# Performance work log

Hardware: AMD Instinct MI355X
Metric: run time of the kernel (lower is better)

## Reference

```python
import jax, jax.numpy as jnp
import numpy as np
import math
from jax import lax

# cfg['MODEL'] constants
MU = 0.1          # FISTA step size
LMBD = 0.1        # LAMBDA[0], sparsity weight
N_DICT = 1        # EXPANSION_FACTOR
N_STEPS = 6       # NUM_LAYERS (FISTA iterations)
K = 3             # kernel_size
PAD = 1           # padding
STRIDE = 1        # stride (POOLING=False, stride passed to conv)
DN = ('NCHW', 'OIHW', 'NCHW')


def _conv(x, w):
    # F.conv2d(x, w, stride=1, padding=PAD)
    return lax.conv_general_dilated(x, w, (STRIDE, STRIDE), [(PAD, PAD), (PAD, PAD)], dimension_numbers=DN)


def _conv_t(y, w):
    # F.conv_transpose2d(y, w, stride=1, padding=PAD) == conv2d with flipped, in/out-swapped kernel, pad K-1-PAD
    wt = jnp.transpose(jnp.flip(w, (-1, -2)), (1, 0, 2, 3))  # [Cin, Cout, K, K]
    p = K - 1 - PAD
    return lax.conv_general_dilated(y, wt, (1, 1), [(p, p), (p, p)], dimension_numbers=DN)


def _shrink(z, thr):
    # non_negative=True soft-threshold: relu(z - thr)
    return jax.nn.relu(z - thr)


def setup_inputs() -> dict:
    key = jax.random.key(0)
    k1, k2 = jax.random.split(key)
    x = jax.random.normal(k1, (16, 64, 56, 56), dtype=jnp.float32)
    # dictionary weight [out_channels, in_channels*n_dict, K, K], kaiming-ish scale
    W = jax.random.normal(k2, (128, 64 * N_DICT, K, K), dtype=jnp.float32) * 0.05
    return {"x": x, "W": W}


def reference(x, W):
    # w_norm: each output filter normalized to unit Frobenius norm
    Wn = W / jnp.sqrt(jnp.sum(W * W, axis=(1, 2, 3), keepdims=True) + 1e-12)
    thr = MU * LMBD
    xr = jnp.tile(x, (1, N_DICT, 1, 1)) if N_DICT > 1 else x

    # FISTA iteration 0: c = shrink(mu * D^T x)
    c = _shrink(MU * _conv(xr, Wn), thr)
    y = c
    c_prev = c
    t = 1.0
    for _ in range(N_STEPS - 1):
        r = xr - _conv_t(y, Wn)                       # residual x - D c
        c_new = _shrink(y + MU * _conv(r, Wn), thr)   # gradient step + shrink
        t_next = (1.0 + math.sqrt(1.0 + 4.0 * t * t)) / 2.0
        y = c_new + ((t - 1.0) / t_next) * (c_new - c_prev)  # momentum
        c_prev = c_new
        t = t_next
    # POOLING=False -> DictConv2d returns the sparse code directly
    return c_prev
```

## Files before the change

kernel.cpp:

```cpp
#include <hip/hip_runtime.h>
#include <hip/hip_bf16.h>
#include <math.h>

typedef __attribute__((ext_vector_type(8))) short short8;
typedef __attribute__((ext_vector_type(16))) float f32x16;

#define MU_  0.1f
#define THR_ 0.01f

static __device__ inline short f2bf(float f) {
    __hip_bfloat16 h = __float2bfloat16(f);
    return *reinterpret_cast<short*>(&h);
}
static __device__ inline float bf2f(unsigned short u) {
    unsigned int x = ((unsigned int)u) << 16;
    return __builtin_bit_cast(float, x);
}

__global__ __launch_bounds__(256) void zero_kernel(float4* p, int n4) {
    int i = blockIdx.x * 256 + threadIdx.x;
    if (i < n4) p[i] = make_float4(0.f, 0.f, 0.f, 0.f);
}

__global__ __launch_bounds__(64) void wnorm_pack(
    const float* __restrict__ W, short* __restrict__ Wf, short* __restrict__ Wt) {
    int co = blockIdx.x, ci = threadIdx.x;
    const float* wp = W + (co * 64 + ci) * 9;
    float v[9]; float s = 0.f;
#pragma unroll
    for (int t = 0; t < 9; ++t) { v[t] = wp[t]; s += v[t] * v[t]; }
#pragma unroll
    for (int off = 32; off; off >>= 1) s += __shfl_xor(s, off, 64);
    float inv = 1.0f / sqrtf(s + 1e-12f);
#pragma unroll
    for (int t = 0; t < 9; ++t) {
        Wf[(t * 128 + co) * 64 + (ci ^ ((co & 7) << 3))] = f2bf(v[t] * inv);
        Wt[(t * 64 + ci) * 128 + (co ^ ((ci & 7) << 3))] = f2bf(v[8 - t] * inv);
    }
}

__global__ __launch_bounds__(256) void pack_x(
    const float* __restrict__ x, short* __restrict__ Xp) {
    __shared__ float lx[64 * 57];
    int row = blockIdx.x, n = blockIdx.y, tid = threadIdx.x;
    short* dst = Xp + ((size_t)(n * 58 + row) * 68) * 64;
    if (row >= 1 && row <= 56) {
        int h = row - 1;
        for (int j = tid; j < 64 * 56; j += 256) {
            int ci = j / 56, w = j - ci * 56;
            lx[ci * 57 + w] = x[((size_t)(n * 64 + ci)) * 3136 + h * 56 + w];
        }
        __syncthreads();
        for (int j = tid; j < 68 * 64; j += 256) {
            int s = j >> 6, ci = j & 63;
            float val = (s >= 2 && s < 58) ? lx[ci * 57 + (s - 2)] : 0.f;
            dst[(s << 6) + (ci ^ ((s & 7) << 3))] = f2bf(val);
        }
    } else {
        for (int j = tid; j < 68 * 64; j += 256) dst[j] = 0;
    }
}

__global__ __launch_bounds__(256) void conv_fwd(
    const short* __restrict__ inp,
    const short* __restrict__ Wf,
    short* __restrict__ Yp,
    short* __restrict__ Cp,
    float* __restrict__ outp, int mode, float beta) {
    __shared__ short xs[3 * 68 * 64];
    const int r = blockIdx.x + 1, cb = blockIdx.y, n = blockIdx.z, tid = threadIdx.x;
    {
        const short8* src = (const short8*)(inp + ((size_t)(n * 58 + (r - 1)) * 68) * 64);
        short8* d = (short8*)xs;
        for (int j = tid; j < 1632; j += 256) d[j] = src[j];
    }

    const size_t prow = ((size_t)(n * 58 + r) * 68) * 128;
    short8 yold8[2], cold8[2];
    int pvv[2], pg[2]; bool pok[2];
#pragma unroll
    for (int k = 0; k < 2; ++k) {
        int item = tid + k * 256;
        pok[k] = item < 448;
        pvv[k] = item >> 3; pg[k] = item & 7;
        if (mode != 0 && pok[k]) {
            int s = pvv[k] + 2;
            size_t off = prow + (size_t)s * 128 + 8 * ((pg[k] + 8 * cb) ^ (s & 7));
            yold8[k] = *(const short8*)(Yp + off);
            if (mode == 1) cold8[k] = *(const short8*)(Cp + off);
        }
    }
    __syncthreads();

    const int lane = tid & 63, wid = tid >> 6, qh = lane >> 5, v0 = lane & 31;
    const int ms = wid & 1, ph = wid >> 1;
    const int co = cb * 64 + ms * 32 + v0;
    const int v  = ph * 32 + v0;
    const int h  = r - 1;

    int goffA[4], bg[3][4];
#pragma unroll
    for (int s = 0; s < 4; ++s) goffA[s] = 8 * ((2 * s + qh) ^ (v0 & 7));
#pragma unroll
    for (int dw = 0; dw < 3; ++dw) {
        int key = (v0 + dw + 1) & 7;
#pragma unroll
        for (int s = 0; s < 4; ++s) bg[dw][s] = 8 * ((2 * s + qh) ^ key);
    }
    const short* wbase = Wf + co * 64;

    f32x16 acc;
#pragma unroll
    for (int i = 0; i < 16; ++i) acc[i] = 0.f;

    short8 Af[2][4];
#pragma unroll
    for (int s = 0; s < 4; ++s) Af[0][s] = *(const short8*)(wbase + goffA[s]);

#pragma unroll
    for (int t = 0; t < 9; ++t) {
        if (t + 1 < 9) {
#pragma unroll
            for (int s = 0; s < 4; ++s)
                Af[(t + 1) & 1][s] = *(const short8*)(wbase + (t + 1) * 8192 + goffA[s]);
        }
        const int dh = t / 3, dw = t % 3;
        const int b_base = (dh * 68 + (v + dw + 1)) * 64;
#pragma unroll
        for (int s = 0; s < 4; ++s) {
            short8 bv = *(const short8*)(xs + b_base + bg[dw][s]);
            acc = __builtin_amdgcn_mfma_f32_32x32x16_bf16(Af[t & 1][s], bv, acc, 0, 0, 0);
        }
    }

    __syncthreads();
    short* tb_y = xs;
    short* tb_c = xs + 4608;
    if (mode != 0) {
#pragma unroll
        for (int k = 0; k < 2; ++k) if (pok[k]) {
            int o = pvv[k] * 72 + 8 * (pg[k] ^ (pvv[k] & 3));
            *(short8*)(tb_y + o) = yold8[k];
            if (mode == 1) *(short8*)(tb_c + o) = cold8[k];
        }
    }
    __syncthreads();
#pragma unroll
    for (int reg = 0; reg < 16; ++reg) {
        const int crl = (reg & 3) + 8 * (reg >> 2) + 4 * qh;
        const int lch = ms * 32 + crl;
        const int slot = v * 72 + (lch ^ ((v & 3) << 3));
        const float a = acc[reg];
        if (mode == 0) {
            float c = fmaxf(MU_ * a - THR_, 0.f);
            short cb16 = f2bf(c);
            tb_y[slot] = cb16;
            tb_c[slot] = cb16;
        } else if (mode == 1) {
            float yold = bf2f((unsigned short)tb_y[slot]);
            float cold = bf2f((unsigned short)tb_c[slot]);
            float c = fmaxf(yold + MU_ * a - THR_, 0.f);
            float ynew = c + beta * (c - cold);
            tb_y[slot] = f2bf(ynew);
            tb_c[slot] = f2bf(c);
        } else {
            if (v < 56) {
                float yold = bf2f((unsigned short)tb_y[slot]);
                float c = fmaxf(yold + MU_ * a - THR_, 0.f);
                outp[((size_t)(n * 128 + cb * 64 + lch)) * 3136 + h * 56 + v] = c;
            }
        }
    }
    if (mode != 2) {
        __syncthreads();
        short* ydst = Yp + prow;
        short* cdst = Cp + prow;
        for (int item = tid; item < 448; item += 256) {
            int vv = item >> 3, g = item & 7;
            int so = vv * 72 + 8 * (g ^ (vv & 3));
            short8 yv = *(const short8*)(tb_y + so);
            short8 cv = *(const short8*)(tb_c + so);
            int s = vv + 2;
            size_t off = (size_t)s * 128 + 8 * ((g + 8 * cb) ^ (s & 7));
            *(short8*)(ydst + off) = yv;
            *(short8*)(cdst + off) = cv;
        }
    }
}

__global__ __launch_bounds__(256) void conv_t(
    const short* __restrict__ Ypb,
    const short* __restrict__ Wt,
    const short* __restrict__ Xp,
    short* __restrict__ Rp) {
    __shared__ short ys[3 * 68 * 128];
    const int r = blockIdx.x + 1, n = blockIdx.y, tid = threadIdx.x;
    {
        const short8* src = (const short8*)(Ypb + ((size_t)(n * 58 + (r - 1)) * 68) * 128);
        short8* d = (short8*)ys;
        for (int j = tid; j < 3264; j += 256) d[j] = src[j];
    }

    const size_t prow = ((size_t)(n * 58 + r) * 68) * 64;
    short8 xold8[2];
    int pvv[2], pg[2]; bool pok[2];
#pragma unroll
    for (int k = 0; k < 2; ++k) {
        int item = tid + k * 256;
        pok[k] = item < 448;
        pvv[k] = item >> 3; pg[k] = item & 7;
        if (pok[k]) {
            int s = pvv[k] + 2;
            xold8[k] = *(const short8*)(Xp + prow + (size_t)s * 64 + 8 * (pg[k] ^ (s & 7)));
        }
    }
    __syncthreads();

    const int lane = tid & 63, wid = tid >> 6, qh = lane >> 5, l31 = lane & 31;
    const int cib = (wid & 1) * 32, vb = (wid >> 1) * 32;
    const int ci = cib + l31;
    const int v = vb + l31;

    int goffA[8], bg[3][8];
#pragma unroll
    for (int s = 0; s < 8; ++s) goffA[s] = 8 * ((2 * s + qh) ^ (ci & 7));
#pragma unroll
    for (int dw = 0; dw < 3; ++dw) {
        int key = (l31 + dw + 1) & 7;
#pragma unroll
        for (int s = 0; s < 8; ++s) bg[dw][s] = 8 * ((2 * s + qh) ^ key);
    }
    const short* wbase = Wt + ci * 128;

    f32x16 acc;
#pragma unroll
    for (int i = 0; i < 16; ++i) acc[i] = 0.f;

    short8 Af[2][8];
#pragma unroll
    for (int s = 0; s < 8; ++s) Af[0][s] = *(const short8*)(wbase + goffA[s]);

#pragma unroll
    for (int t = 0; t < 9; ++t) {
        if (t + 1 < 9) {
#pragma unroll
            for (int s = 0; s < 8; ++s)
                Af[(t + 1) & 1][s] = *(const short8*)(wbase + (t + 1) * 8192 + goffA[s]);
        }
        const int dh = t / 3, dw = t % 3;
        const int b_base = (dh * 68 + (v + dw + 1)) * 128;
#pragma unroll
        for (int s = 0; s < 8; ++s) {
            short8 bv = *(const short8*)(ys + b_base + bg[dw][s]);
            acc = __builtin_amdgcn_mfma_f32_32x32x16_bf16(Af[t & 1][s], bv, acc, 0, 0, 0);
        }
    }

    __syncthreads();
    short* tb = ys;
#pragma unroll
    for (int k = 0; k < 2; ++k) if (pok[k]) {
        *(short8*)(tb + pvv[k] * 72 + 8 * (pg[k] ^ (pvv[k] & 3))) = xold8[k];
    }
    __syncthreads();
#pragma unroll
    for (int reg = 0; reg < 16; ++reg) {
        const int cir = cib + (reg & 3) + 8 * (reg >> 2) + 4 * qh;
        const int slot = v * 72 + (cir ^ ((v & 3) << 3));
        float xo = bf2f((unsigned short)tb[slot]);
        tb[slot] = f2bf(xo - acc[reg]);
    }
    __syncthreads();
    short* rdst = Rp + prow;
    for (int item = tid; item < 448; item += 256) {
        int vv = item >> 3, g = item & 7;
        short8 val = *(const short8*)(tb + vv * 72 + 8 * (g ^ (vv & 3)));
        int s = vv + 2;
        *(short8*)(rdst + (size_t)s * 64 + 8 * (g ^ (s & 7))) = val;
    }
}

extern "C" void kernel_launch(void* const* d_in, const int* in_sizes, int n_in,
                              void* d_out, int out_size, void* d_ws, size_t ws_size,
                              hipStream_t stream) {
    const float* x = (const float*)d_in[0];
    const float* W = (const float*)d_in[1];
    float* out = (float*)d_out;

    const size_t XPN = (size_t)16 * 58 * 68 * 64;
    const size_t YPN = 2 * XPN;
    short* Xp = (short*)d_ws;
    short* Rp = Xp + XPN;
    short* Yp = Rp + XPN;
    short* Cp = Yp + YPN;
    short* Wf = Cp + YPN;
    short* Wt = Wf + 9 * 128 * 64;

    const int n4 = (int)((XPN + YPN) * 2 / 16);
    hipLaunchKernelGGL(zero_kernel, dim3((n4 + 255) / 256), dim3(256), 0, stream,
                       (float4*)Rp, n4);
    hipLaunchKernelGGL(wnorm_pack, dim3(128), dim3(64), 0, stream, W, Wf, Wt);
    hipLaunchKernelGGL(pack_x, dim3(58, 16), dim3(256), 0, stream, x, Xp);

    dim3 gf(56, 2, 16), gt(56, 16), b(256, 1, 1);
    hipLaunchKernelGGL(conv_fwd, gf, b, 0, stream, Xp, Wf, Yp, Cp,
                       (float*)nullptr, 0, 0.f);
    double t = 1.0;
    for (int it = 1; it <= 5; ++it) {
        hipLaunchKernelGGL(conv_t, gt, b, 0, stream, Yp, Wt, Xp, Rp);
        double tn = (1.0 + sqrt(1.0 + 4.0 * t * t)) / 2.0;
        float beta = (float)((t - 1.0) / tn);
        hipLaunchKernelGGL(conv_fwd, gf, b, 0, stream, Rp, Wf, Yp, Cp,
                           (it == 5) ? out : (float*)nullptr, (it == 5) ? 2 : 1,
                           beta);
        t = tn;
    }
}
```

Baseline: 406.1 us.

## Merge output-channel blocks in conv_fwd and stage weights through shared memory

conv_fwd now runs one 512-thread block per output row that computes all 128 output channels, where before two 256-thread blocks each handled 64 channels. The input row tile is loaded into shared memory once per row instead of twice. Weights are repacked into an MFMA-friendly layout and double-buffered in LDS: each tap's weights are loaded cooperatively, replacing per-lane global loads. This adds a __syncthreads per tap, raises LDS use to about 58KB per block, and halves the grid, which may lower occupancy.

```diff
diff --git a/kernel.cpp b/kernel.cpp
--- a/kernel.cpp
+++ b/kernel.cpp
@@ -23,7 +23,7 @@
 }
 
 __global__ __launch_bounds__(64) void wnorm_pack(
-    const float* __restrict__ W, short* __restrict__ Wf, short* __restrict__ Wt) {
+    const float* __restrict__ W, short* __restrict__ Wf2, short* __restrict__ Wt) {
     int co = blockIdx.x, ci = threadIdx.x;
     const float* wp = W + (co * 64 + ci) * 9;
     float v[9]; float s = 0.f;
@@ -34,7 +34,7 @@
     float inv = 1.0f / sqrtf(s + 1e-12f);
 #pragma unroll
     for (int t = 0; t < 9; ++t) {
-        Wf[(t * 128 + co) * 64 + (ci ^ ((co & 7) << 3))] = f2bf(v[t] * inv);
+        Wf2[((t * 8 + (ci >> 3)) * 128 + co) * 8 + (ci & 7)] = f2bf(v[t] * inv);
         Wt[(t * 64 + ci) * 128 + (co ^ ((ci & 7) << 3))] = f2bf(v[8 - t] * inv);
     }
 }
@@ -61,85 +61,92 @@
     }
 }
 
-__global__ __launch_bounds__(256) void conv_fwd(
+__global__ __launch_bounds__(512, 4) void conv_fwd(
     const short* __restrict__ inp,
-    const short* __restrict__ Wf,
+    const short* __restrict__ Wf2,
     short* __restrict__ Yp,
     short* __restrict__ Cp,
     float* __restrict__ outp, int mode, float beta) {
-    __shared__ short xs[3 * 68 * 64];
-    const int r = blockIdx.x + 1, cb = blockIdx.y, n = blockIdx.z, tid = threadIdx.x;
+    __shared__ __align__(16) short smem[29440];
+    short* xs = smem;
+    short* a0 = smem + 13056;
+    short* a1 = smem + 21248;
+    const int r = blockIdx.x + 1, n = blockIdx.y, tid = threadIdx.x;
+
+    const size_t prow = ((size_t)(n * 58 + r) * 68) * 128;
+    short8 yold8[2], cold8[2];
+    int pvv[2], pg[2]; bool pok[2];
+#pragma unroll
+    for (int k = 0; k < 2; ++k) {
+        int item = tid + k * 512;
+        pok[k] = item < 896;
+        pvv[k] = item >> 4; pg[k] = item & 15;
+        if (mode != 0 && pok[k]) {
+            int s = pvv[k] + 2;
+            size_t off = prow + (size_t)s * 128 + 8 * (pg[k] ^ (s & 7));
+            yold8[k] = *(const short8*)(Yp + off);
+            if (mode == 1) cold8[k] = *(const short8*)(Cp + off);
+        }
+    }
     {
         const short8* src = (const short8*)(inp + ((size_t)(n * 58 + (r - 1)) * 68) * 64);
         short8* d = (short8*)xs;
-        for (int j = tid; j < 1632; j += 256) d[j] = src[j];
-    }
-
-    const size_t prow = ((size_t)(n * 58 + r) * 68) * 128;
-    short8 yold8[2], cold8[2];
-    int pvv[2], pg[2]; bool pok[2];
-#pragma unroll
-    for (int k = 0; k < 2; ++k) {
-        int item = tid + k * 256;
-        pok[k] = item < 448;
-        pvv[k] = item >> 3; pg[k] = item & 7;
-        if (mode != 0 && pok[k]) {
-            int s = pvv[k] + 2;
-            size_t off = prow + (size_t)s * 128 + 8 * ((pg[k] + 8 * cb) ^ (s & 7));
-            yold8[k] = *(const short8*)(Yp + off);
-            if (mode == 1) cold8[k] = *(const short8*)(Cp + off);
-        }
+        for (int j = tid; j < 1632; j += 512) d[j] = src[j];
+    }
+    {
+        const short8* asrc = (const short8*)Wf2;
+        short8 s0 = asrc[tid], s1 = asrc[tid + 512];
+        ((short8*)a0)[tid] = s0; ((short8*)a0)[tid + 512] = s1;
     }
     __syncthreads();
 
     const int lane = tid & 63, wid = tid >> 6, qh = lane >> 5, v0 = lane & 31;
-    const int ms = wid & 1, ph = wid >> 1;
-    const int co = cb * 64 + ms * 32 + v0;
+    const int cot = wid & 3, ph = wid >> 2;
+    const int co = cot * 32 + v0;
     const int v  = ph * 32 + v0;
     const int h  = r - 1;
 
-    int goffA[4], bg[3][4];
-#pragma unroll
-    for (int s = 0; s < 4; ++s) goffA[s] = 8 * ((2 * s + qh) ^ (v0 & 7));
+    int bg[3][4];
 #pragma unroll
     for (int dw = 0; dw < 3; ++dw) {
         int key = (v0 + dw + 1) & 7;
 #pragma unroll
         for (int s = 0; s < 4; ++s) bg[dw][s] = 8 * ((2 * s + qh) ^ key);
     }
-    const short* wbase = Wf + co * 64;
 
     f32x16 acc;
 #pragma unroll
     for (int i = 0; i < 16; ++i) acc[i] = 0.f;
 
-    short8 Af[2][4];
-#pragma unroll
-    for (int s = 0; s < 4; ++s) Af[0][s] = *(const short8*)(wbase + goffA[s]);
-
 #pragma unroll
     for (int t = 0; t < 9; ++t) {
-        if (t + 1 < 9) {
-#pragma unroll
-            for (int s = 0; s < 4; ++s)
-                Af[(t + 1) & 1][s] = *(const short8*)(wbase + (t + 1) * 8192 + goffA[s]);
+        short8 st0, st1;
+        if (t < 8) {
+            const short8* asrc = (const short8*)(Wf2 + (t + 1) * 8192);
+            st0 = asrc[tid]; st1 = asrc[tid + 512];
         }
         const int dh = t / 3, dw = t % 3;
         const int b_base = (dh * 68 + (v + dw + 1)) * 64;
+        const short* abuf = (t & 1) ? a1 : a0;
 #pragma unroll
         for (int s = 0; s < 4; ++s) {
-            short8 bv = *(const short8*)(xs + b_base + bg[dw][s]);
-            acc = __builtin_amdgcn_mfma_f32_32x32x16_bf16(Af[t & 1][s], bv, acc, 0, 0, 0);
-        }
-    }
-
-    __syncthreads();
-    short* tb_y = xs;
-    short* tb_c = xs + 4608;
+            short8 aF = *(const short8*)(abuf + ((2 * s + qh) * 128 + co) * 8);
+            short8 bF = *(const short8*)(xs + b_base + bg[dw][s]);
+            acc = __builtin_amdgcn_mfma_f32_32x32x16_bf16(aF, bF, acc, 0, 0, 0);
+        }
+        if (t < 8) {
+            short8* ad = (short8*)((t & 1) ? a0 : a1);
+            ad[tid] = st0; ad[tid + 512] = st1;
+        }
+        __syncthreads();
+    }
+
+    short* tb_y = smem;
+    short* tb_c = smem + 8704;
     if (mode != 0) {
 #pragma unroll
         for (int k = 0; k < 2; ++k) if (pok[k]) {
-            int o = pvv[k] * 72 + 8 * (pg[k] ^ (pvv[k] & 3));
+            int o = pvv[k] * 136 + 8 * (pg[k] ^ (pvv[k] & 3));
             *(short8*)(tb_y + o) = yold8[k];
             if (mode == 1) *(short8*)(tb_c + o) = cold8[k];
         }
@@ -148,8 +155,8 @@
 #pragma unroll
     for (int reg = 0; reg < 16; ++reg) {
         const int crl = (reg & 3) + 8 * (reg >> 2) + 4 * qh;
-        const int lch = ms * 32 + crl;
-        const int slot = v * 72 + (lch ^ ((v & 3) << 3));
+        const int lch = cot * 32 + crl;
+        const int slot = v * 136 + (lch ^ ((v & 3) << 3));
         const float a = acc[reg];
         if (mode == 0) {
             float c = fmaxf(MU_ * a - THR_, 0.f);
@@ -167,23 +174,21 @@
             if (v < 56) {
                 float yold = bf2f((unsigned short)tb_y[slot]);
                 float c = fmaxf(yold + MU_ * a - THR_, 0.f);
-                outp[((size_t)(n * 128 + cb * 64 + lch)) * 3136 + h * 56 + v] = c;
+                outp[((size_t)(n * 128 + lch)) * 3136 + h * 56 + v] = c;
             }
         }
     }
     if (mode != 2) {
         __syncthreads();
-        short* ydst = Yp + prow;
-        short* cdst = Cp + prow;
-        for (int item = tid; item < 448; item += 256) {
-            int vv = item >> 3, g = item & 7;
-            int so = vv * 72 + 8 * (g ^ (vv & 3));
+        for (int item = tid; item < 896; item += 512) {
+            int vv = item >> 4, g = item & 15;
+            int so = vv * 136 + 8 * (g ^ (vv & 3));
             short8 yv = *(const short8*)(tb_y + so);
             short8 cv = *(const short8*)(tb_c + so);
             int s = vv + 2;
-            size_t off = (size_t)s * 128 + 8 * ((g + 8 * cb) ^ (s & 7));
-            *(short8*)(ydst + off) = yv;
-            *(short8*)(cdst + off) = cv;
+            size_t off = prow + (size_t)s * 128 + 8 * (g ^ (s & 7));
+            *(short8*)(Yp + off) = yv;
+            *(short8*)(Cp + off) = cv;
         }
     }
 }
@@ -293,24 +298,24 @@
     short* Rp = Xp + XPN;
     short* Yp = Rp + XPN;
     short* Cp = Yp + YPN;
-    short* Wf = Cp + YPN;
-    short* Wt = Wf + 9 * 128 * 64;
+    short* Wf2 = Cp + YPN;
+    short* Wt  = Wf2 + 73728;
 
     const int n4 = (int)((XPN + YPN) * 2 / 16);
     hipLaunchKernelGGL(zero_kernel, dim3((n4 + 255) / 256), dim3(256), 0, stream,
                        (float4*)Rp, n4);
-    hipLaunchKernelGGL(wnorm_pack, dim3(128), dim3(64), 0, stream, W, Wf, Wt);
+    hipLaunchKernelGGL(wnorm_pack, dim3(128), dim3(64), 0, stream, W, Wf2, Wt);
     hipLaunchKernelGGL(pack_x, dim3(58, 16), dim3(256), 0, stream, x, Xp);
 
-    dim3 gf(56, 2, 16), gt(56, 16), b(256, 1, 1);
-    hipLaunchKernelGGL(conv_fwd, gf, b, 0, stream, Xp, Wf, Yp, Cp,
+    dim3 gf(56, 16), gt(56, 16);
+    hipLaunchKernelGGL(conv_fwd, gf, dim3(512), 0, stream, Xp, Wf2, Yp, Cp,
                        (float*)nullptr, 0, 0.f);
     double t = 1.0;
     for (int it = 1; it <= 5; ++it) {
-        hipLaunchKernelGGL(conv_t, gt, b, 0, stream, Yp, Wt, Xp, Rp);
+        hipLaunchKernelGGL(conv_t, gt, dim3(256), 0, stream, Yp, Wt, Xp, Rp);
         double tn = (1.0 + sqrt(1.0 + 4.0 * t * t)) / 2.0;
         float beta = (float)((t - 1.0) / tn);
-        hipLaunchKernelGGL(conv_fwd, gf, b, 0, stream, Rp, Wf, Yp, Cp,
+        hipLaunchKernelGGL(conv_fwd, gf, dim3(512), 0, stream, Rp, Wf2, Yp, Cp,
                            (it == 5) ? out : (float*)nullptr, (it == 5) ? 2 : 1,
                            beta);
         t = tn;
```

Measured after the change: 429.5 us. 5.8% more time.

## Switch convs to 16x16x32 MFMA with register-resident weights and padded LDS rows

Applied to the files above, without the earlier changes.

Both convolution kernels move from 32x32x16 MFMA with double-buffered weight fragments to 16x16x32 MFMA, where each wave owns 16 output channels across four 16-pixel tiles. All 18 weight fragments are loaded into registers up front from a new channel-blocked weight layout. Input rows are staged into LDS with a 72-short padded stride, and conv_t processes its 128 input channels in two 64-channel passes so it can share the same smaller LDS buffer. The aim is more B-operand reuse per weight load and less LDS. The cost is more registers from holding all weight fragments at once, which could limit occupancy, and an extra barrier in conv_t.

```diff
diff --git a/kernel.cpp b/kernel.cpp
--- a/kernel.cpp
+++ b/kernel.cpp
@@ -3,7 +3,7 @@
 #include <math.h>
 
 typedef __attribute__((ext_vector_type(8))) short short8;
-typedef __attribute__((ext_vector_type(16))) float f32x16;
+typedef __attribute__((ext_vector_type(4))) float f32x4;
 
 #define MU_  0.1f
 #define THR_ 0.01f
@@ -23,7 +23,7 @@
 }
 
 __global__ __launch_bounds__(64) void wnorm_pack(
-    const float* __restrict__ W, short* __restrict__ Wf, short* __restrict__ Wt) {
+    const float* __restrict__ W, short* __restrict__ Wf2, short* __restrict__ Wt2) {
     int co = blockIdx.x, ci = threadIdx.x;
     const float* wp = W + (co * 64 + ci) * 9;
     float v[9]; float s = 0.f;
@@ -34,8 +34,8 @@
     float inv = 1.0f / sqrtf(s + 1e-12f);
 #pragma unroll
     for (int t = 0; t < 9; ++t) {
-        Wf[(t * 128 + co) * 64 + (ci ^ ((co & 7) << 3))] = f2bf(v[t] * inv);
-        Wt[(t * 64 + ci) * 128 + (co ^ ((ci & 7) << 3))] = f2bf(v[8 - t] * inv);
+        Wf2[((t * 8 + (ci >> 3)) * 128 + co) * 8 + (ci & 7)] = f2bf(v[t] * inv);
+        Wt2[((t * 16 + (co >> 3)) * 64 + ci) * 8 + (co & 7)] = f2bf(v[8 - t] * inv);
     }
 }
 
@@ -63,220 +63,179 @@
 
 __global__ __launch_bounds__(256) void conv_fwd(
     const short* __restrict__ inp,
-    const short* __restrict__ Wf,
+    const short* __restrict__ Wf2,
     short* __restrict__ Yp,
     short* __restrict__ Cp,
     float* __restrict__ outp, int mode, float beta) {
-    __shared__ short xs[3 * 68 * 64];
+    __shared__ __align__(16) short smem[14688];
     const int r = blockIdx.x + 1, cb = blockIdx.y, n = blockIdx.z, tid = threadIdx.x;
     {
         const short8* src = (const short8*)(inp + ((size_t)(n * 58 + (r - 1)) * 68) * 64);
-        short8* d = (short8*)xs;
-        for (int j = tid; j < 1632; j += 256) d[j] = src[j];
-    }
-
+        for (int j = tid; j < 1632; j += 256) {
+            int srow = j >> 3, w = j & 7;
+            *(short8*)(smem + srow * 72 + w * 8) = src[j];
+        }
+    }
+    const int lane = tid & 63, ct = tid >> 6, quad = lane >> 4, l15 = lane & 15;
+    const int co = cb * 64 + ct * 16 + l15;
+
+    short8 Areg[18];
+#pragma unroll
+    for (int f = 0; f < 18; ++f) {
+        int t = f >> 1, half = f & 1;
+        Areg[f] = *(const short8*)(Wf2 + ((size_t)((t * 8 + half * 4 + quad) * 128 + co)) * 8);
+    }
+    __syncthreads();
+
+    f32x4 acc[4];
+#pragma unroll
+    for (int pt = 0; pt < 4; ++pt) acc[pt] = (f32x4){0.f, 0.f, 0.f, 0.f};
+
+#pragma unroll
+    for (int f = 0; f < 18; ++f) {
+        const int t = f >> 1, half = f & 1;
+        const int dh = t / 3, dw = t % 3;
+        const int u = l15 + dw + 1;
+        const int phys = (half * 4 + quad) ^ (u & 7);
+        const int base = (dh * 68 + u) * 72 + phys * 8;
+#pragma unroll
+        for (int pt = 0; pt < 4; ++pt) {
+            short8 bv = *(const short8*)(smem + base + pt * 1152);
+            acc[pt] = __builtin_amdgcn_mfma_f32_16x16x32_bf16(Areg[f], bv, acc[pt], 0, 0, 0);
+        }
+    }
+
+    __syncthreads();
+    short* tb_y = smem;
+    short* tb_c = smem + 4608;
     const size_t prow = ((size_t)(n * 58 + r) * 68) * 128;
-    short8 yold8[2], cold8[2];
-    int pvv[2], pg[2]; bool pok[2];
-#pragma unroll
-    for (int k = 0; k < 2; ++k) {
-        int item = tid + k * 256;
-        pok[k] = item < 448;
-        pvv[k] = item >> 3; pg[k] = item & 7;
-        if (mode != 0 && pok[k]) {
-            int s = pvv[k] + 2;
-            size_t off = prow + (size_t)s * 128 + 8 * ((pg[k] + 8 * cb) ^ (s & 7));
-            yold8[k] = *(const short8*)(Yp + off);
-            if (mode == 1) cold8[k] = *(const short8*)(Cp + off);
-        }
-    }
-    __syncthreads();
-
-    const int lane = tid & 63, wid = tid >> 6, qh = lane >> 5, v0 = lane & 31;
-    const int ms = wid & 1, ph = wid >> 1;
-    const int co = cb * 64 + ms * 32 + v0;
-    const int v  = ph * 32 + v0;
-    const int h  = r - 1;
-
-    int goffA[4], bg[3][4];
-#pragma unroll
-    for (int s = 0; s < 4; ++s) goffA[s] = 8 * ((2 * s + qh) ^ (v0 & 7));
-#pragma unroll
-    for (int dw = 0; dw < 3; ++dw) {
-        int key = (v0 + dw + 1) & 7;
-#pragma unroll
-        for (int s = 0; s < 4; ++s) bg[dw][s] = 8 * ((2 * s + qh) ^ key);
-    }
-    const short* wbase = Wf + co * 64;
-
-    f32x16 acc;
-#pragma unroll
-    for (int i = 0; i < 16; ++i) acc[i] = 0.f;
-
-    short8 Af[2][4];
-#pragma unroll
-    for (int s = 0; s < 4; ++s) Af[0][s] = *(const short8*)(wbase + goffA[s]);
-
-#pragma unroll
-    for (int t = 0; t < 9; ++t) {
-        if (t + 1 < 9) {
-#pragma unroll
-            for (int s = 0; s < 4; ++s)
-                Af[(t + 1) & 1][s] = *(const short8*)(wbase + (t + 1) * 8192 + goffA[s]);
-        }
-        const int dh = t / 3, dw = t % 3;
-        const int b_base = (dh * 68 + (v + dw + 1)) * 64;
-#pragma unroll
-        for (int s = 0; s < 4; ++s) {
-            short8 bv = *(const short8*)(xs + b_base + bg[dw][s]);
-            acc = __builtin_amdgcn_mfma_f32_32x32x16_bf16(Af[t & 1][s], bv, acc, 0, 0, 0);
-        }
-    }
-
-    __syncthreads();
-    short* tb_y = xs;
-    short* tb_c = xs + 4608;
     if (mode != 0) {
-#pragma unroll
-        for (int k = 0; k < 2; ++k) if (pok[k]) {
-            int o = pvv[k] * 72 + 8 * (pg[k] ^ (pvv[k] & 3));
-            *(short8*)(tb_y + o) = yold8[k];
-            if (mode == 1) *(short8*)(tb_c + o) = cold8[k];
-        }
-    }
-    __syncthreads();
-#pragma unroll
-    for (int reg = 0; reg < 16; ++reg) {
-        const int crl = (reg & 3) + 8 * (reg >> 2) + 4 * qh;
-        const int lch = ms * 32 + crl;
-        const int slot = v * 72 + (lch ^ ((v & 3) << 3));
-        const float a = acc[reg];
-        if (mode == 0) {
-            float c = fmaxf(MU_ * a - THR_, 0.f);
-            short cb16 = f2bf(c);
-            tb_y[slot] = cb16;
-            tb_c[slot] = cb16;
-        } else if (mode == 1) {
-            float yold = bf2f((unsigned short)tb_y[slot]);
-            float cold = bf2f((unsigned short)tb_c[slot]);
-            float c = fmaxf(yold + MU_ * a - THR_, 0.f);
-            float ynew = c + beta * (c - cold);
-            tb_y[slot] = f2bf(ynew);
-            tb_c[slot] = f2bf(c);
-        } else {
-            if (v < 56) {
+        for (int item = tid; item < 448; item += 256) {
+            int vv = item >> 3, g = item & 7;
+            int s = vv + 2;
+            size_t off = prow + (size_t)s * 128 + 8 * ((g + 8 * cb) ^ (s & 7));
+            int o = vv * 72 + 8 * (g ^ (vv & 3));
+            *(short8*)(tb_y + o) = *(const short8*)(Yp + off);
+            if (mode == 1) *(short8*)(tb_c + o) = *(const short8*)(Cp + off);
+        }
+    }
+    __syncthreads();
+    const int h = r - 1;
+#pragma unroll
+    for (int pt = 0; pt < 4; ++pt) {
+        const int px = pt * 16 + l15;
+#pragma unroll
+        for (int reg = 0; reg < 4; ++reg) {
+            const int lch = ct * 16 + quad * 4 + reg;
+            const int slot = px * 72 + (lch ^ ((px & 3) << 3));
+            const float a = acc[pt][reg];
+            if (mode == 0) {
+                float c = fmaxf(MU_ * a - THR_, 0.f);
+                short cb16 = f2bf(c);
+                tb_y[slot] = cb16;
+                tb_c[slot] = cb16;
+            } else if (mode == 1) {
                 float yold = bf2f((unsigned short)tb_y[slot]);
+                float cold = bf2f((unsigned short)tb_c[slot]);
                 float c = fmaxf(yold + MU_ * a - THR_, 0.f);
-                outp[((size_t)(n * 128 + cb * 64 + lch)) * 3136 + h * 56 + v] = c;
+                tb_y[slot] = f2bf(c + beta * (c - cold));
+                tb_c[slot] = f2bf(c);
+            } else {
+                if (px < 56) {
+                    float yold = bf2f((unsigned short)tb_y[slot]);
+                    float c = fmaxf(yold + MU_ * a - THR_, 0.f);
+                    outp[((size_t)(n * 128 + cb * 64 + lch)) * 3136 + h * 56 + px] = c;
+                }
             }
         }
     }
     if (mode != 2) {
         __syncthreads();
-        short* ydst = Yp + prow;
-        short* cdst = Cp + prow;
         for (int item = tid; item < 448; item += 256) {
             int vv = item >> 3, g = item & 7;
             int so = vv * 72 + 8 * (g ^ (vv & 3));
             short8 yv = *(const short8*)(tb_y + so);
             short8 cv = *(const short8*)(tb_c + so);
             int s = vv + 2;
-            size_t off = (size_t)s * 128 + 8 * ((g + 8 * cb) ^ (s & 7));
-            *(short8*)(ydst + off) = yv;
-            *(short8*)(cdst + off) = cv;
+            size_t off = prow + (size_t)s * 128 + 8 * ((g + 8 * cb) ^ (s & 7));
+            *(short8*)(Yp + off) = yv;
+            *(short8*)(Cp + off) = cv;
         }
     }
 }
 
 __global__ __launch_bounds__(256) void conv_t(
     const short* __restrict__ Ypb,
-    const short* __restrict__ Wt,
+    const short* __restrict__ Wt2,
     const short* __restrict__ Xp,
     short* __restrict__ Rp) {
-    __shared__ short ys[3 * 68 * 128];
+    __shared__ __align__(16) short smem[14688];
     const int r = blockIdx.x + 1, n = blockIdx.y, tid = threadIdx.x;
-    {
-        const short8* src = (const short8*)(Ypb + ((size_t)(n * 58 + (r - 1)) * 68) * 128);
-        short8* d = (short8*)ys;
-        for (int j = tid; j < 3264; j += 256) d[j] = src[j];
-    }
-
+    const int lane = tid & 63, ct = tid >> 6, quad = lane >> 4, l15 = lane & 15;
+    const int ci = ct * 16 + l15;
+    const short8* src = (const short8*)(Ypb + ((size_t)(n * 58 + (r - 1)) * 68) * 128);
+
+    f32x4 acc[4];
+#pragma unroll
+    for (int pt = 0; pt < 4; ++pt) acc[pt] = (f32x4){0.f, 0.f, 0.f, 0.f};
+
+#pragma unroll
+    for (int p = 0; p < 2; ++p) {
+        if (p) __syncthreads();
+        for (int j = tid; j < 1632; j += 256) {
+            int srow = j >> 3, w = j & 7;
+            *(short8*)(smem + srow * 72 + w * 8) = src[srow * 16 + p * 8 + w];
+        }
+        short8 Areg[18];
+#pragma unroll
+        for (int f = 0; f < 18; ++f) {
+            int t = f >> 1, sh = f & 1;
+            Areg[f] = *(const short8*)(Wt2 +
+                ((size_t)((t * 16 + (p * 2 + sh) * 4 + quad) * 64 + ci)) * 8);
+        }
+        __syncthreads();
+#pragma unroll
+        for (int f = 0; f < 18; ++f) {
+            const int t = f >> 1, sh = f & 1;
+            const int dh = t / 3, dw = t % 3;
+            const int u = l15 + dw + 1;
+            const int phys = (sh * 4 + quad) ^ (u & 7);
+            const int base = (dh * 68 + u) * 72 + phys * 8;
+#pragma unroll
+            for (int pt = 0; pt < 4; ++pt) {
+                short8 bv = *(const short8*)(smem + base + pt * 1152);
+                acc[pt] = __builtin_amdgcn_mfma_f32_16x16x32_bf16(Areg[f], bv, acc[pt], 0, 0, 0);
+            }
+        }
+    }
+
+    __syncthreads();
+    short* tb = smem;
     const size_t prow = ((size_t)(n * 58 + r) * 68) * 64;
-    short8 xold8[2];
-    int pvv[2], pg[2]; bool pok[2];
-#pragma unroll
-    for (int k = 0; k < 2; ++k) {
-        int item = tid + k * 256;
-        pok[k] = item < 448;
-        pvv[k] = item >> 3; pg[k] = item & 7;
-        if (pok[k]) {
-            int s = pvv[k] + 2;
-            xold8[k] = *(const short8*)(Xp + prow + (size_t)s * 64 + 8 * (pg[k] ^ (s & 7)));
-        }
-    }
-    __syncthreads();
-
-    const int lane = tid & 63, wid = tid >> 6, qh = lane >> 5, l31 = lane & 31;
-    const int cib = (wid & 1) * 32, vb = (wid >> 1) * 32;
-    const int ci = cib + l31;
-    const int v = vb + l31;
-
-    int goffA[8], bg[3][8];
-#pragma unroll
-    for (int s = 0; s < 8; ++s) goffA[s] = 8 * ((2 * s + qh) ^ (ci & 7));
-#pragma unroll
-    for (int dw = 0; dw < 3; ++dw) {
-        int key = (l31 + dw + 1) & 7;
-#pragma unroll
-        for (int s = 0; s < 8; ++s) bg[dw][s] = 8 * ((2 * s + qh) ^ key);
-    }
-    const short* wbase = Wt + ci * 128;
-
-    f32x16 acc;
-#pragma unroll
-    for (int i = 0; i < 16; ++i) acc[i] = 0.f;
-
-    short8 Af[2][8];
-#pragma unroll
-    for (int s = 0; s < 8; ++s) Af[0][s] = *(const short8*)(wbase + goffA[s]);
-
-#pragma unroll
-    for (int t = 0; t < 9; ++t) {
-        if (t + 1 < 9) {
-#pragma unroll
-            for (int s = 0; s < 8; ++s)
-                Af[(t + 1) & 1][s] = *(const short8*)(wbase + (t + 1) * 8192 + goffA[s]);
-        }
-        const int dh = t / 3, dw = t % 3;
-        const int b_base = (dh * 68 + (v + dw + 1)) * 128;
-#pragma unroll
-        for (int s = 0; s < 8; ++s) {
-            short8 bv = *(const short8*)(ys + b_base + bg[dw][s]);
-            acc = __builtin_amdgcn_mfma_f32_32x32x16_bf16(Af[t & 1][s], bv, acc, 0, 0, 0);
-        }
-    }
-
-    __syncthreads();
-    short* tb = ys;
-#pragma unroll
-    for (int k = 0; k < 2; ++k) if (pok[k]) {
-        *(short8*)(tb + pvv[k] * 72 + 8 * (pg[k] ^ (pvv[k] & 3))) = xold8[k];
-    }
-    __syncthreads();
-#pragma unroll
-    for (int reg = 0; reg < 16; ++reg) {
-        const int cir = cib + (reg & 3) + 8 * (reg >> 2) + 4 * qh;
-        const int slot = v * 72 + (cir ^ ((v & 3) << 3));
-        float xo = bf2f((unsigned short)tb[slot]);
-        tb[slot] = f2bf(xo - acc[reg]);
-    }
-    __syncthreads();
-    short* rdst = Rp + prow;
+    for (int item = tid; item < 448; item += 256) {
+        int vv = item >> 3, g = item & 7;
+        int s = vv + 2;
+        *(short8*)(tb + vv * 72 + 8 * (g ^ (vv & 3))) =
+            *(const short8*)(Xp + prow + (size_t)s * 64 + 8 * (g ^ (s & 7)));
+    }
+    __syncthreads();
+#pragma unroll
+    for (int pt = 0; pt < 4; ++pt) {
+        const int px = pt * 16 + l15;
+#pragma unroll
+        for (int reg = 0; reg < 4; ++reg) {
+            const int cir = ct * 16 + quad * 4 + reg;
+            const int slot = px * 72 + (cir ^ ((px & 3) << 3));
+            float xo = bf2f((unsigned short)tb[slot]);
+            tb[slot] = f2bf(xo - acc[pt][reg]);
+        }
+    }
+    __syncthreads();
     for (int item = tid; item < 448; item += 256) {
         int vv = item >> 3, g = item & 7;
         short8 val = *(const short8*)(tb + vv * 72 + 8 * (g ^ (vv & 3)));
         int s = vv + 2;
-        *(short8*)(rdst + (size_t)s * 64 + 8 * (g ^ (s & 7))) = val;
+        *(short8*)(Rp + prow + (size_t)s * 64 + 8 * (g ^ (s & 7))) = val;
     }
 }
 
@@ -293,24 +252,24 @@
     short* Rp = Xp + XPN;
     short* Yp = Rp + XPN;
     short* Cp = Yp + YPN;
-    short* Wf = Cp + YPN;
-    short* Wt = Wf + 9 * 128 * 64;
+    short* Wf2 = Cp + YPN;
+    short* Wt2 = Wf2 + 73728;
 
     const int n4 = (int)((XPN + YPN) * 2 / 16);
     hipLaunchKernelGGL(zero_kernel, dim3((n4 + 255) / 256), dim3(256), 0, stream,
                        (float4*)Rp, n4);
-    hipLaunchKernelGGL(wnorm_pack, dim3(128), dim3(64), 0, stream, W, Wf, Wt);
+    hipLaunchKernelGGL(wnorm_pack, dim3(128), dim3(64), 0, stream, W, Wf2, Wt2);
     hipLaunchKernelGGL(pack_x, dim3(58, 16), dim3(256), 0, stream, x, Xp);
 
     dim3 gf(56, 2, 16), gt(56, 16), b(256, 1, 1);
-    hipLaunchKernelGGL(conv_fwd, gf, b, 0, stream, Xp, Wf, Yp, Cp,
+    hipLaunchKernelGGL(conv_fwd, gf, b, 0, stream, Xp, Wf2, Yp, Cp,
                        (float*)nullptr, 0, 0.f);
     double t = 1.0;
     for (int it = 1; it <= 5; ++it) {
-        hipLaunchKernelGGL(conv_t, gt, b, 0, stream, Yp, Wt, Xp, Rp);
+        hipLaunchKernelGGL(conv_t, gt, b, 0, stream, Yp, Wt2, Xp, Rp);
         double tn = (1.0 + sqrt(1.0 + 4.0 * t * t)) / 2.0;
         float beta = (float)((t - 1.0) / tn);
-        hipLaunchKernelGGL(conv_fwd, gf, b, 0, stream, Rp, Wf, Yp, Cp,
+        hipLaunchKernelGGL(conv_fwd, gf, b, 0, stream, Rp, Wf2, Yp, Cp,
                            (it == 5) ? out : (float*)nullptr, (it == 5) ? 2 : 1,
                            beta);
         t = tn;
```

After: 372.4 us. 1.09x faster.
